# Optimization experiments

Hardware: AMD Instinct MI355X
Metric: run time of the kernel (lower is better)

## Reference

```python
import jax, jax.numpy as jnp
import numpy as np

B, N, H, F, DIN, NC = 4, 1024, 8, 256, 256, 10  # batch graphs, nodes, heads, feat/head, input dim, classes


def setup_inputs() -> dict:
    key = jax.random.key(0)
    ks = jax.random.split(key, 12)
    def rn(k, shape, s=0.05):
        return jax.random.normal(k, shape, jnp.float32) * s
    return dict(
        features=rn(ks[0], (B, N, DIN), 1.0),
        eigvects=rn(ks[1], (B, N, DIN), 1.0),  # unused by forward, mirrors original signature
        attn_mask=jnp.zeros((B, N, N), jnp.float32),  # additive mask: 0 = edge, -inf = no edge
        W1=rn(ks[2], (DIN, H * F)), a_src1=rn(ks[3], (H, F)), a_tgt1=rn(ks[4], (H, F)),
        skip1=rn(ks[5], (DIN, H * F)), b1=jnp.zeros((H * F,), jnp.float32),
        W2=rn(ks[6], (H * F, H * F)), a_src2=rn(ks[7], (H, F)), a_tgt2=rn(ks[8], (H, F)),
        skip2=rn(ks[9], (H * F, H * F)), b2=jnp.zeros((F,), jnp.float32),
        Wc=rn(ks[10], (F, NC)), bc=jnp.zeros((NC,), jnp.float32),
    )


def _gat_layer(x, mask, W, a_s, a_t, skipW, b, concat):
    # GAT IMP2: dense all-pairs scores + additive connectivity mask. Dropout is eval-mode identity.
    Bb, Nn, _ = x.shape
    Hh, Ff = a_s.shape
    p = (x @ W).reshape(Bb, Nn, Hh, Ff)                      # projected node features (B,N,H,F)
    s_src = jnp.einsum('bnhf,hf->bnh', p, a_s)
    s_tgt = jnp.einsum('bnhf,hf->bnh', p, a_t)
    # score[b,i,j,h] = leaky(src_i + tgt_j) + mask[b,i,j]
    scores = jax.nn.leaky_relu(s_src[:, :, None, :] + s_tgt[:, None, :, :], 0.2) + mask[..., None]
    attn = jax.nn.softmax(scores, axis=2)                    # softmax over neighbors j
    out = jnp.einsum('bijh,bjhf->bihf', attn, p)
    out = out + (x @ skipW).reshape(Bb, Nn, Hh, Ff)          # skip connection (projected)
    out = out.reshape(Bb, Nn, Hh * Ff) if concat else out.mean(axis=2)
    out = out + b
    return jax.nn.elu(out) if concat else out


def reference(features, eigvects, attn_mask, W1, a_src1, a_tgt1, skip1, b1,
              W2, a_src2, a_tgt2, skip2, b2, Wc, bc):
    x = _gat_layer(features, attn_mask, W1, a_src1, a_tgt1, skip1, b1, True)   # (B,N,H*F), ELU
    x = _gat_layer(x, attn_mask, W2, a_src2, a_tgt2, skip2, b2, False)         # (B,N,F), heads averaged
    g = x.mean(axis=1)                                                         # mean pool over nodes
    return g @ Wc + bc                                                         # (B, n_classes)
```

## Files before the change

### kernel.cpp

```cpp
#include <hip/hip_runtime.h>
#include <hip/hip_bf16.h>
#include <stdint.h>
#include <stddef.h>

typedef __hip_bfloat16 bf16;
typedef __attribute__((ext_vector_type(8))) short bhalf8;
typedef __attribute__((ext_vector_type(4))) short short4v;
typedef __attribute__((ext_vector_type(4))) float floatx4;

static __device__ __forceinline__ float b2f(bf16 v) { return __bfloat162float(v); }
static __device__ __forceinline__ bf16  f2b(float v) { return __float2bfloat16(v); }
static __device__ __forceinline__ short f2s(float v) {
    union { bf16 b; short s; } u; u.b = __float2bfloat16(v); return u.s;
}
static __device__ __forceinline__ float s2f(short v) {
    union { short s; bf16 b; } u; u.s = v; return b2f(u.b);
}

static __device__ __forceinline__ float loadf(const void* p, size_t i, int f32) {
    return f32 ? ((const float*)p)[i] : b2f(((const bf16*)p)[i]);
}

static __device__ __forceinline__ void gl_lds16(const void* g, void* l) {
    __builtin_amdgcn_global_load_lds(
        (const __attribute__((address_space(1))) void*)g,
        (__attribute__((address_space(3))) void*)l, 16, 0, 0);
}

static __device__ __forceinline__ void load_mask4(const void* mask, size_t idx,
                                                  int f32, float* mv) {
    if (f32) {
        float4 v = *(const float4*)((const float*)mask + idx);
        mv[0] = v.x; mv[1] = v.y; mv[2] = v.z; mv[3] = v.w;
    } else {
        const bf16* p = (const bf16*)mask + idx;
        #pragma unroll
        for (int t = 0; t < 4; t++) mv[t] = b2f(p[t]);
    }
}

__global__ __launch_bounds__(256) void prep_k(const void* __restrict__ feat,
                                              bf16* __restrict__ featc,
                                              float* __restrict__ zbase, int nzero,
                                              const void* __restrict__ W1,
                                              bf16* __restrict__ W1t,
                                              const void* __restrict__ skip1,
                                              bf16* __restrict__ S1t,
                                              const void* __restrict__ W2,
                                              const void* __restrict__ a_src1,
                                              const void* __restrict__ a_tgt1,
                                              const void* __restrict__ a_src2,
                                              const void* __restrict__ a_tgt2,
                                              bf16* __restrict__ Wa1b,
                                              bf16* __restrict__ Wa2b,
                                              int* __restrict__ flagp)
{
    __shared__ int sflag;
    __shared__ bf16 tile[32][33];
    const int tid = threadIdx.x;

    if (tid < 64) {
        const unsigned short* s = (const unsigned short*)W1;
        int bad = 0;
        #pragma unroll
        for (int i = 0; i < 4; i++) {
            int e = (s[tid * 4 + i] >> 7) & 0xFF;
            if (e > 0x85 || (e != 0 && e < 0x60)) bad++;
        }
        bad += __shfl_xor(bad, 1, 64);
        bad += __shfl_xor(bad, 2, 64);
        bad += __shfl_xor(bad, 4, 64);
        bad += __shfl_xor(bad, 8, 64);
        bad += __shfl_xor(bad, 16, 64);
        bad += __shfl_xor(bad, 32, 64);
        if (tid == 0) sflag = (bad > 16) ? 1 : 0;
    }
    __syncthreads();
    const int f32 = sflag;

    int id = blockIdx.x;
    if (id == 0 && tid == 0) *flagp = f32;

    if (id < 4096) {
        const int i = id * 256 + tid;
        featc[i] = f32 ? f2b(((const float*)feat)[i]) : ((const bf16*)feat)[i];
        return;
    }
    id -= 4096;
    if (id < 480) {
        const int i = id * 256 + tid;
        if (i < nzero) zbase[i] = 0.f;
        return;
    }
    id -= 480;
    if (id < 1024) {
        const void* in = (id < 512) ? W1 : skip1;
        bf16* out = (id < 512) ? W1t : S1t;
        const int t = id & 511;
        const int bx = t & 63, byy = t >> 6;
        const int tx = tid & 31, ty = tid >> 5;
        const int c0 = bx * 32, r0 = byy * 32;
        #pragma unroll
        for (int yy = ty; yy < 32; yy += 8)
            tile[yy][tx] = f2b(loadf(in, (size_t)(r0 + yy) * 2048 + c0 + tx, f32));
        __syncthreads();
        #pragma unroll
        for (int yy = ty; yy < 32; yy += 8)
            out[(size_t)(c0 + yy) * 256 + r0 + tx] = tile[tx][yy];
        return;
    }
    id -= 1024;
    if (id < 128) {
        const int wave = tid >> 6, lane = tid & 63;
        const int base = id * 256;
        const int hh = base >> 11, h = hh & 7;
        const void* a = (hh < 8) ? a_src2 : a_tgt2;
        float av[4];
        #pragma unroll
        for (int i = 0; i < 4; i++) av[i] = loadf(a, h * 256 + lane * 4 + i, f32);
        for (int o = 0; o < 64; o++) {
            const int idx = base + wave * 64 + o;
            const int k = idx & 2047;
            float acc = 0.f;
            #pragma unroll
            for (int i = 0; i < 4; i++)
                acc = fmaf(loadf(W2, (size_t)k * 2048 + h * 256 + lane * 4 + i, f32),
                           av[i], acc);
            #pragma unroll
            for (int off2 = 32; off2; off2 >>= 1) acc += __shfl_down(acc, off2, 64);
            if (lane == 0) Wa2b[idx] = f2b(acc);
        }
        return;
    }
    id -= 128;
    {
        const int wave = tid >> 6, lane = tid & 63;
        const int base = id * 256;
        const int hh = base >> 8, h = hh & 7;
        const void* a = (hh < 8) ? a_src1 : a_tgt1;
        float av[4];
        #pragma unroll
        for (int i = 0; i < 4; i++) av[i] = loadf(a, h * 256 + lane * 4 + i, f32);
        for (int o = 0; o < 64; o++) {
            const int idx = base + wave * 64 + o;
            const int k = idx & 255;
            float acc = 0.f;
            #pragma unroll
            for (int i = 0; i < 4; i++)
                acc = fmaf(loadf(W1, (size_t)k * 2048 + h * 256 + lane * 4 + i, f32),
                           av[i], acc);
            #pragma unroll
            for (int off2 = 32; off2; off2 >>= 1) acc += __shfl_down(acc, off2, 64);
            if (lane == 0) Wa1b[idx] = f2b(acc);
        }
    }
}

__global__ __launch_bounds__(256) void gemm_dual(const bf16* __restrict__ featc,
                                                 const bf16* __restrict__ W1t,
                                                 const bf16* __restrict__ S1t,
                                                 bf16* __restrict__ pT,
                                                 bf16* __restrict__ sk1)
{
    __shared__ __align__(16) short sA[128][32];
    __shared__ __align__(16) short sB[128][32];
    const int tid = threadIdx.x;
    const int z = blockIdx.z;
    const bf16* A  = z ? featc : W1t;
    const bf16* Bt = z ? S1t   : featc;
    const int mbase = (z ? blockIdx.x : blockIdx.y) * 128;
    const int nbase = (z ? blockIdx.y : blockIdx.x) * 128;
    const int wave = tid >> 6, lane = tid & 63;
    const int wm = wave >> 1, wn = wave & 1;
    const int lrow = lane & 15, quad = lane >> 4;

    floatx4 acc[4][4];
    #pragma unroll
    for (int i = 0; i < 4; i++)
        #pragma unroll
        for (int j = 0; j < 4; j++)
            acc[i][j] = (floatx4){0.f, 0.f, 0.f, 0.f};

    const int srow = wave * 32 + (lane >> 2);
    const int scol = (lane & 3) * 8;
    const bf16* gA0 = A  + (size_t)(mbase + srow) * 256 + scol;
    const bf16* gA1 = gA0 + (size_t)16 * 256;
    const bf16* gB0 = Bt + (size_t)(nbase + srow) * 256 + scol;
    const bf16* gB1 = gB0 + (size_t)16 * 256;
    char* lA0 = (char*)&sA[0][0] + wave * 2048 + lane * 16;
    char* lA1 = lA0 + 1024;
    char* lB0 = (char*)&sB[0][0] + wave * 2048 + lane * 16;
    char* lB1 = lB0 + 1024;

    for (int k0 = 0; k0 < 256; k0 += 32) {
        __syncthreads();
        gl_lds16(gA0 + k0, lA0);
        gl_lds16(gA1 + k0, lA1);
        gl_lds16(gB0 + k0, lB0);
        gl_lds16(gB1 + k0, lB1);
        __syncthreads();
        bhalf8 af[4], bfr[4];
        #pragma unroll
        for (int t = 0; t < 4; t++) af[t]  = *(const bhalf8*)&sA[wm * 64 + t * 16 + lrow][quad * 8];
        #pragma unroll
        for (int t = 0; t < 4; t++) bfr[t] = *(const bhalf8*)&sB[wn * 64 + t * 16 + lrow][quad * 8];
        #pragma unroll
        for (int tm = 0; tm < 4; tm++)
            #pragma unroll
            for (int tn = 0; tn < 4; tn++)
                acc[tm][tn] = __builtin_amdgcn_mfma_f32_16x16x32_bf16(af[tm], bfr[tn], acc[tm][tn], 0, 0, 0);
    }

    #pragma unroll
    for (int tm = 0; tm < 4; tm++) {
        #pragma unroll
        for (int tn = 0; tn < 4; tn++) {
            const int col = nbase + wn * 64 + tn * 16 + lrow;
            #pragma unroll
            for (int r = 0; r < 4; r++) {
                const int row = mbase + wm * 64 + tm * 16 + quad * 4 + r;
                if (z) {
                    sk1[(size_t)row * 2048 + col] = f2b(acc[tm][tn][r]);
                } else {
                    const size_t idx = ((size_t)((col >> 10) * 8 + (row >> 8)) << 18)
                                     + (size_t)(row & 255) * 1024 + (col & 1023);
                    pT[idx] = f2b(acc[tm][tn][r]);
                }
            }
        }
    }
}

template <int K>
__global__ __launch_bounds__(256) void score_k(const bf16* __restrict__ X,
                                               const bf16* __restrict__ Wab,
                                               float* __restrict__ ss,
                                               float* __restrict__ st)
{
    constexpr int VPL = K / 64;
    const int wave = threadIdx.x >> 6, lane = threadIdx.x & 63;
    const int n = blockIdx.x * 4 + wave;
    const int b = n >> 10, nn = n & 1023;

    const bf16* xr = X + (size_t)n * K + lane * VPL;
    float xv[VPL];
    if (VPL == 4) {
        short4v v = *(const short4v*)xr;
        #pragma unroll
        for (int t = 0; t < 4; t++) xv[t] = s2f(v[t]);
    } else {
        #pragma unroll
        for (int c = 0; c < VPL / 8; c++) {
            bhalf8 v = *(const bhalf8*)(xr + c * 8);
            #pragma unroll
            for (int t = 0; t < 8; t++) xv[c * 8 + t] = s2f(v[t]);
        }
    }

    #pragma unroll
    for (int hh = 0; hh < 16; hh++) {
        const bf16* wr = Wab + (size_t)hh * K + lane * VPL;
        float acc = 0.f;
        if (VPL == 4) {
            short4v v = *(const short4v*)wr;
            #pragma unroll
            for (int t = 0; t < 4; t++) acc = fmaf(xv[t], s2f(v[t]), acc);
        } else {
            #pragma unroll
            for (int c = 0; c < VPL / 8; c++) {
                bhalf8 v = *(const bhalf8*)(wr + c * 8);
                #pragma unroll
                for (int t = 0; t < 8; t++) acc = fmaf(xv[c * 8 + t], s2f(v[t]), acc);
            }
        }
        #pragma unroll
        for (int off = 32; off; off >>= 1) acc += __shfl_down(acc, off, 64);
        if (lane == 0) {
            const int h = hh & 7;
            if (hh < 8) ss[(b * 8 + h) * 1024 + nn] = acc;
            else        st[(b * 8 + h) * 1024 + nn] = acc;
        }
    }
}

__global__ __launch_bounds__(256) void attn_fused(const float* __restrict__ s_src_t,
                                                  const float* __restrict__ s_tgt_t,
                                                  const void* __restrict__ mask,
                                                  const bf16* __restrict__ pT,
                                                  const bf16* __restrict__ sk,
                                                  const void* __restrict__ bias,
                                                  bf16* __restrict__ x2,
                                                  const int* __restrict__ flag)
{
    __shared__ __align__(16) short sA[2][32][32];
    __shared__ __align__(16) short sB[2][256][32];
    __shared__ short sStgt[1024];
    __shared__ float sInvl[32];

    const int tid = threadIdx.x;
    const int by = blockIdx.x, bh = blockIdx.y;
    const int b = bh >> 3, h = bh & 7;
    const int f32 = *flag;
    const int wave = tid >> 6, lane = tid & 63;
    const int lrow = lane & 15, quad = lane >> 4;

    #pragma unroll
    for (int q = 0; q < 4; q++)
        sStgt[q * 256 + tid] = f2s(s_tgt_t[bh * 1024 + q * 256 + tid]);

    const int row  = tid >> 3;
    const int col0 = (tid & 7) * 4;
    const float ssr = s_src_t[bh * 1024 + by * 32 + row];
    const size_t mrow0 = ((size_t)(b * 1024 + by * 32 + row)) << 10;

    const bf16* gB = pT + ((size_t)bh << 18) + (size_t)(tid >> 2) * 1024 + (tid & 3) * 8;

    floatx4 acc[2][4];
    #pragma unroll
    for (int i = 0; i < 2; i++)
        #pragma unroll
        for (int j = 0; j < 4; j++)
            acc[i][j] = (floatx4){0.f, 0.f, 0.f, 0.f};

    float lacc = 0.f;

    auto stageB = [&](int k0, int buf) {
        const bf16* g = gB + k0;
        char* l = (char*)&sB[buf][0][0] + tid * 16;
        #pragma unroll
        for (int c = 0; c < 4; c++)
            gl_lds16(g + (size_t)(64 * c) * 1024, l + c * 4096);
    };
    auto genA = [&](int k0, int buf, const float* mv) {
        const short* sp = &sStgt[k0 + col0];
        short4v ev;
        #pragma unroll
        for (int t = 0; t < 4; t++) {
            float x = ssr + s2f(sp[t]);
            x = fmaxf(x, 0.2f * x);
            float e = __expf(x + mv[t]);
            lacc += e;
            ev[t] = f2s(e);
        }
        *(short4v*)&sA[buf][row][col0] = ev;
    };

    float mv[4];
    stageB(0, 0);
    load_mask4(mask, mrow0 + col0, f32, mv);
    __syncthreads();
    genA(0, 0, mv);
    load_mask4(mask, mrow0 + 32 + col0, f32, mv);

    int cur = 0;
    for (int k0 = 0; k0 < 1024; k0 += 32, cur ^= 1) {
        __syncthreads();
        if (k0 + 32 < 1024) {
            const int nxt = cur ^ 1;
            stageB(k0 + 32, nxt);
            genA(k0 + 32, nxt, mv);
            if (k0 + 64 < 1024)
                load_mask4(mask, mrow0 + k0 + 64 + col0, f32, mv);
        }
        bhalf8 af[2], bfr[4];
        #pragma unroll
        for (int mt = 0; mt < 2; mt++)
            af[mt] = *(const bhalf8*)&sA[cur][mt * 16 + lrow][quad * 8];
        #pragma unroll
        for (int nt = 0; nt < 4; nt++)
            bfr[nt] = *(const bhalf8*)&sB[cur][wave * 64 + nt * 16 + lrow][quad * 8];
        #pragma unroll
        for (int mt = 0; mt < 2; mt++)
            #pragma unroll
            for (int nt = 0; nt < 4; nt++)
                acc[mt][nt] = __builtin_amdgcn_mfma_f32_16x16x32_bf16(af[mt], bfr[nt], acc[mt][nt], 0, 0, 0);
    }

    lacc += __shfl_xor(lacc, 1, 64);
    lacc += __shfl_xor(lacc, 2, 64);
    lacc += __shfl_xor(lacc, 4, 64);
    if ((tid & 7) == 0) sInvl[row] = 1.0f / lacc;
    __syncthreads();

    #pragma unroll
    for (int mt = 0; mt < 2; mt++) {
        #pragma unroll
        for (int r = 0; r < 4; r++) {
            const int rl = mt * 16 + quad * 4 + r;
            const int rg = by * 32 + rl;
            const float il = sInvl[rl];
            #pragma unroll
            for (int nt = 0; nt < 4; nt++) {
                const int col = wave * 64 + nt * 16 + lrow;
                const int hf = h * 256 + col;
                const size_t idx = ((size_t)(b * 1024 + rg)) * 2048 + hf;
                float v = acc[mt][nt][r] * il + b2f(sk[idx]) + loadf(bias, hf, f32);
                v = (v > 0.f) ? v : expm1f(v);
                x2[idx] = f2b(v);
            }
        }
    }
}

__global__ __launch_bounds__(256) void colsoft_k(const float* __restrict__ s_src_t,
                                                 const float* __restrict__ s_tgt_t,
                                                 const void* __restrict__ mask,
                                                 float* __restrict__ c,
                                                 const int* __restrict__ flagp)
{
    __shared__ float sS[64];
    __shared__ float sIl[64];
    const int f32 = *flagp;
    const int bh = blockIdx.x, iz = blockIdx.y, b = bh >> 3;
    const int tid = threadIdx.x;
    const int i0 = iz * 64;
    if (tid < 64) sS[tid] = s_src_t[bh * 1024 + i0 + tid];
    __syncthreads();

    {
        const int row = tid >> 2, c4 = tid & 3;
        const float ssr = sS[row];
        const size_t mrow = ((size_t)(b * 1024 + i0 + row)) << 10;
        float l = 0.f;
        #pragma unroll 4
        for (int q = 0; q < 64; q++) {
            const int j = c4 * 256 + q * 4;
            float mv[4];
            load_mask4(mask, mrow + j, f32, mv);
            float4 s4 = *(const float4*)(s_tgt_t + bh * 1024 + j);
            float sv[4] = {s4.x, s4.y, s4.z, s4.w};
            #pragma unroll
            for (int t = 0; t < 4; t++) {
                float x = ssr + sv[t];
                x = fmaxf(x, 0.2f * x);
                l += __expf(x + mv[t]);
            }
        }
        l += __shfl_xor(l, 1, 64);
        l += __shfl_xor(l, 2, 64);
        if ((tid & 3) == 0) sIl[row] = 1.0f / l;
    }
    __syncthreads();

    const int j0 = tid * 4;
    float4 s4 = *(const float4*)(s_tgt_t + bh * 1024 + j0);
    float sv[4] = {s4.x, s4.y, s4.z, s4.w};
    float a[4] = {0.f, 0.f, 0.f, 0.f};
    #pragma unroll 4
    for (int r = 0; r < 64; r++) {
        const float sr = sS[r], il = sIl[r];
        float mv[4];
        load_mask4(mask, (((size_t)(b * 1024 + i0 + r)) << 10) + j0, f32, mv);
        #pragma unroll
        for (int t = 0; t < 4; t++) {
            float x = sr + sv[t];
            x = fmaxf(x, 0.2f * x);
            a[t] = fmaf(il, __expf(x + mv[t]), a[t]);
        }
    }
    #pragma unroll
    for (int t = 0; t < 4; t++)
        atomicAdd(&c[bh * 1024 + j0 + t], a[t]);
}

__global__ __launch_bounds__(256) void yx_k(const bf16* __restrict__ x2,
                                            const float* __restrict__ c,
                                            float* __restrict__ y,
                                            float* __restrict__ xbar)
{
    __shared__ float sC[8][128];
    const int b = blockIdx.x, kt = blockIdx.y, jc = blockIdx.z;
    const int t = threadIdx.x;
    const int k = kt * 256 + t;
    const int j0 = jc * 128;
    for (int idx = t; idx < 8 * 128; idx += 256) {
        const int h = idx >> 7, jj = idx & 127;
        sC[h][jj] = c[(b * 8 + h) * 1024 + j0 + jj];
    }
    __syncthreads();
    float acc[8] = {0.f, 0.f, 0.f, 0.f, 0.f, 0.f, 0.f, 0.f};
    float ax = 0.f;
    for (int jj = 0; jj < 128; jj++) {
        const float xv = b2f(x2[((size_t)(b * 1024 + j0 + jj)) * 2048 + k]);
        ax += xv;
        #pragma unroll
        for (int h = 0; h < 8; h++) acc[h] = fmaf(sC[h][jj], xv, acc[h]);
    }
    #pragma unroll
    for (int h = 0; h < 8; h++)
        atomicAdd(&y[(b * 8 + h) * 2048 + k], acc[h]);
    atomicAdd(&xbar[b * 2048 + k], ax);
}

__global__ __launch_bounds__(256) void gs_k(const void* __restrict__ W2,
                                            const void* __restrict__ skip2,
                                            const float* __restrict__ y,
                                            const float* __restrict__ xbar,
                                            float* __restrict__ gA,
                                            float* __restrict__ gS,
                                            const int* __restrict__ flagp)
{
    __shared__ float sY[256];
    const int f32 = *flagp;
    int id = blockIdx.x;
    if (id < 256) {
        const int bh = id & 31, kc = id >> 5;
        const int h = bh & 7, f = threadIdx.x;
        const int k0 = kc * 256;
        sY[threadIdx.x] = y[bh * 2048 + k0 + threadIdx.x];
        __syncthreads();
        float acc = 0.f;
        #pragma unroll 4
        for (int kk = 0; kk < 256; kk++)
            acc = fmaf(sY[kk], loadf(W2, (size_t)(k0 + kk) * 2048 + h * 256 + f, f32), acc);
        atomicAdd(&gA[bh * 256 + f], acc);
    } else {
        const int idx = id - 256;
        const int b = idx & 3, hft = (idx >> 2) & 7, kc = idx >> 5;
        const int hf = hft * 256 + threadIdx.x;
        float acc = 0.f;
        #pragma unroll 4
        for (int kk = 0; kk < 256; kk++) {
            const int k = kc * 256 + kk;
            acc = fmaf(xbar[b * 2048 + k], loadf(skip2, (size_t)k * 2048 + hf, f32), acc);
        }
        atomicAdd(&gS[b * 2048 + hf], acc);
    }
}

__global__ __launch_bounds__(256) void classify2_k(const float* __restrict__ gA,
                                                   const float* __restrict__ gS,
                                                   const void* __restrict__ b2,
                                                   const void* __restrict__ Wc,
                                                   const void* __restrict__ bc,
                                                   void* __restrict__ out,
                                                   const int* __restrict__ flag)
{
    __shared__ float gv[256];
    const int f32 = *flag;
    const int b = blockIdx.x, f = threadIdx.x;
    float s = 0.f;
    #pragma unroll
    for (int h = 0; h < 8; h++)
        s += gA[(b * 8 + h) * 256 + f] + gS[b * 2048 + h * 256 + f];
    gv[f] = s * (1.0f / 8192.0f) + loadf(b2, f, f32);
    __syncthreads();
    if (f < 10) {
        float acc = loadf(bc, f, f32);
        for (int k = 0; k < 256; k++)
            acc = fmaf(gv[k], loadf(Wc, k * 10 + f, f32), acc);
        if (f32) ((float*)out)[b * 10 + f] = acc;
        else     ((bf16*)out)[b * 10 + f] = f2b(acc);
    }
}

extern "C" void kernel_launch(void* const* d_in, const int* in_sizes, int n_in,
                              void* d_out, int out_size, void* d_ws, size_t ws_size,
                              hipStream_t stream)
{
    (void)in_sizes; (void)n_in; (void)out_size; (void)ws_size;
    const void* feat   = d_in[0];
    const void* mask   = d_in[2];
    const void* W1     = d_in[3];
    const void* a_src1 = d_in[4];
    const void* a_tgt1 = d_in[5];
    const void* skip1  = d_in[6];
    const void* b1     = d_in[7];
    const void* W2     = d_in[8];
    const void* a_src2 = d_in[9];
    const void* a_tgt2 = d_in[10];
    const void* skip2  = d_in[11];
    const void* b2v    = d_in[12];
    const void* Wc     = d_in[13];
    const void* bc     = d_in[14];

    char* ws = (char*)d_ws;
    size_t off = 0;
    auto alloc = [&](size_t bytes) -> void* {
        void* p = ws + off;
        off += (bytes + 255) & ~(size_t)255;
        return p;
    };
    int*   flag  = (int*)alloc(256);
    bf16*  featc = (bf16*)alloc(4096ull * 256 * 2);
    bf16*  W1t   = (bf16*)alloc(2048ull * 256 * 2);
    bf16*  S1t   = (bf16*)alloc(2048ull * 256 * 2);
    bf16*  sk1   = (bf16*)alloc(4096ull * 2048 * 2);
    bf16*  x2    = (bf16*)alloc(4096ull * 2048 * 2);
    bf16*  pT    = (bf16*)alloc(4096ull * 2048 * 2);
    float* ss    = (float*)alloc(32ull * 1024 * 4);
    float* st    = (float*)alloc(32ull * 1024 * 4);
    bf16*  Wa1b  = (bf16*)alloc(16ull * 256 * 2);
    bf16*  Wa2b  = (bf16*)alloc(16ull * 2048 * 2);
    float* cbuf = (float*)alloc(32ull * 1024 * 4);
    float* gA   = (float*)alloc(32ull * 256 * 4);
    float* gS   = (float*)alloc(4ull * 2048 * 4);
    float* xbar = (float*)alloc(4ull * 2048 * 4);
    float* y    = (float*)alloc(32ull * 2048 * 4);
    const int nzero = 32768 + 3 * 8192 + 65536;

    prep_k<<<5744, 256, 0, stream>>>(feat, featc, cbuf, nzero, W1, W1t,
                                     skip1, S1t, W2, a_src1, a_tgt1,
                                     a_src2, a_tgt2, Wa1b, Wa2b, flag);
    gemm_dual<<<dim3(32, 16, 2), 256, 0, stream>>>(featc, W1t, S1t, pT, sk1);
    score_k<256><<<1024, 256, 0, stream>>>(featc, Wa1b, ss, st);
    attn_fused<<<dim3(32, 32), 256, 0, stream>>>(ss, st, mask, pT, sk1, b1, x2, flag);
    score_k<2048><<<1024, 256, 0, stream>>>(x2, Wa2b, ss, st);
    colsoft_k<<<dim3(32, 16), 256, 0, stream>>>(ss, st, mask, cbuf, flag);
    yx_k<<<dim3(4, 8, 8), 256, 0, stream>>>(x2, cbuf, y, xbar);
    gs_k<<<512, 256, 0, stream>>>(W2, skip2, y, xbar, gA, gS, flag);
    classify2_k<<<4, 256, 0, stream>>>(gA, gS, b2v, Wc, bc, d_out, flag);
}
```

Baseline: 400.0 us.

## Pre-convert mask to bf16 and widen grids for prep, yx and gs kernels

Adds a prep stage that converts the additive mask to a bf16 copy, so attn_fused and colsoft_k read it with 8-byte vector loads and half the bytes, with no runtime dtype branch. The Wa1/Wa2 precompute, yx_k and gs_k are split into more blocks over smaller chunks to raise parallelism on long serial loops. gs_k now stages xbar in shared memory. In exchange there is an extra full pass over the mask in prep and more atomicAdd traffic from the finer splits.

After: 350.0 us. -12.5%, faster.

```diff
diff --git a/kernel.cpp b/kernel.cpp
--- a/kernel.cpp
+++ b/kernel.cpp
@@ -27,20 +27,17 @@
         (__attribute__((address_space(3))) void*)l, 16, 0, 0);
 }
 
-static __device__ __forceinline__ void load_mask4(const void* mask, size_t idx,
-                                                  int f32, float* mv) {
-    if (f32) {
-        float4 v = *(const float4*)((const float*)mask + idx);
-        mv[0] = v.x; mv[1] = v.y; mv[2] = v.z; mv[3] = v.w;
-    } else {
-        const bf16* p = (const bf16*)mask + idx;
-        #pragma unroll
-        for (int t = 0; t < 4; t++) mv[t] = b2f(p[t]);
-    }
+static __device__ __forceinline__ void load_mask4b(const bf16* m, size_t idx,
+                                                   float* mv) {
+    short4v v = *(const short4v*)(m + idx);
+    #pragma unroll
+    for (int t = 0; t < 4; t++) mv[t] = s2f(v[t]);
 }
 
 __global__ __launch_bounds__(256) void prep_k(const void* __restrict__ feat,
                                               bf16* __restrict__ featc,
+                                              const void* __restrict__ mask,
+                                              bf16* __restrict__ maskb,
                                               float* __restrict__ zbase, int nzero,
                                               const void* __restrict__ W1,
                                               bf16* __restrict__ W1t,
@@ -87,6 +84,19 @@
         return;
     }
     id -= 4096;
+    if (id < 4096) {
+        const size_t i = (size_t)id * 1024 + tid * 4;
+        if (f32) {
+            float4 v = *(const float4*)((const float*)mask + i);
+            short4v o;
+            o[0] = f2s(v.x); o[1] = f2s(v.y); o[2] = f2s(v.z); o[3] = f2s(v.w);
+            *(short4v*)(maskb + i) = o;
+        } else {
+            *(short4v*)(maskb + i) = *(const short4v*)((const bf16*)mask + i);
+        }
+        return;
+    }
+    id -= 4096;
     if (id < 480) {
         const int i = id * 256 + tid;
         if (i < nzero) zbase[i] = 0.f;
@@ -110,16 +120,17 @@
         return;
     }
     id -= 1024;
-    if (id < 128) {
+    if (id < 512) {
         const int wave = tid >> 6, lane = tid & 63;
-        const int base = id * 256;
+        const int base = id * 64;
         const int hh = base >> 11, h = hh & 7;
         const void* a = (hh < 8) ? a_src2 : a_tgt2;
         float av[4];
         #pragma unroll
         for (int i = 0; i < 4; i++) av[i] = loadf(a, h * 256 + lane * 4 + i, f32);
-        for (int o = 0; o < 64; o++) {
-            const int idx = base + wave * 64 + o;
+        #pragma unroll 4
+        for (int o = 0; o < 16; o++) {
+            const int idx = base + wave * 16 + o;
             const int k = idx & 2047;
             float acc = 0.f;
             #pragma unroll
@@ -132,17 +143,18 @@
         }
         return;
     }
-    id -= 128;
+    id -= 512;
     {
         const int wave = tid >> 6, lane = tid & 63;
-        const int base = id * 256;
+        const int base = id * 64;
         const int hh = base >> 8, h = hh & 7;
         const void* a = (hh < 8) ? a_src1 : a_tgt1;
         float av[4];
         #pragma unroll
         for (int i = 0; i < 4; i++) av[i] = loadf(a, h * 256 + lane * 4 + i, f32);
-        for (int o = 0; o < 64; o++) {
-            const int idx = base + wave * 64 + o;
+        #pragma unroll 4
+        for (int o = 0; o < 16; o++) {
+            const int idx = base + wave * 16 + o;
             const int k = idx & 255;
             float acc = 0.f;
             #pragma unroll
@@ -285,7 +297,7 @@
 
 __global__ __launch_bounds__(256) void attn_fused(const float* __restrict__ s_src_t,
                                                   const float* __restrict__ s_tgt_t,
-                                                  const void* __restrict__ mask,
+                                                  const bf16* __restrict__ maskb,
                                                   const bf16* __restrict__ pT,
                                                   const bf16* __restrict__ sk,
                                                   const void* __restrict__ bias,
@@ -347,10 +359,10 @@
 
     float mv[4];
     stageB(0, 0);
-    load_mask4(mask, mrow0 + col0, f32, mv);
+    load_mask4b(maskb, mrow0 + col0, mv);
     __syncthreads();
     genA(0, 0, mv);
-    load_mask4(mask, mrow0 + 32 + col0, f32, mv);
+    load_mask4b(maskb, mrow0 + 32 + col0, mv);
 
     int cur = 0;
     for (int k0 = 0; k0 < 1024; k0 += 32, cur ^= 1) {
@@ -360,7 +372,7 @@
             stageB(k0 + 32, nxt);
             genA(k0 + 32, nxt, mv);
             if (k0 + 64 < 1024)
-                load_mask4(mask, mrow0 + k0 + 64 + col0, f32, mv);
+                load_mask4b(maskb, mrow0 + k0 + 64 + col0, mv);
         }
         bhalf8 af[2], bfr[4];
         #pragma unroll
@@ -404,13 +416,11 @@
 
 __global__ __launch_bounds__(256) void colsoft_k(const float* __restrict__ s_src_t,
                                                  const float* __restrict__ s_tgt_t,
-                                                 const void* __restrict__ mask,
-                                                 float* __restrict__ c,
-                                                 const int* __restrict__ flagp)
+                                                 const bf16* __restrict__ maskb,
+                                                 float* __restrict__ c)
 {
     __shared__ float sS[64];
     __shared__ float sIl[64];
-    const int f32 = *flagp;
     const int bh = blockIdx.x, iz = blockIdx.y, b = bh >> 3;
     const int tid = threadIdx.x;
     const int i0 = iz * 64;
@@ -426,7 +436,7 @@
         for (int q = 0; q < 64; q++) {
             const int j = c4 * 256 + q * 4;
             float mv[4];
-            load_mask4(mask, mrow + j, f32, mv);
+            load_mask4b(maskb, mrow + j, mv);
             float4 s4 = *(const float4*)(s_tgt_t + bh * 1024 + j);
             float sv[4] = {s4.x, s4.y, s4.z, s4.w};
             #pragma unroll
@@ -450,7 +460,7 @@
     for (int r = 0; r < 64; r++) {
         const float sr = sS[r], il = sIl[r];
         float mv[4];
-        load_mask4(mask, (((size_t)(b * 1024 + i0 + r)) << 10) + j0, f32, mv);
+        load_mask4b(maskb, (((size_t)(b * 1024 + i0 + r)) << 10) + j0, mv);
         #pragma unroll
         for (int t = 0; t < 4; t++) {
             float x = sr + sv[t];
@@ -468,19 +478,20 @@
                                             float* __restrict__ y,
                                             float* __restrict__ xbar)
 {
-    __shared__ float sC[8][128];
+    __shared__ float sC[8][32];
     const int b = blockIdx.x, kt = blockIdx.y, jc = blockIdx.z;
     const int t = threadIdx.x;
     const int k = kt * 256 + t;
-    const int j0 = jc * 128;
-    for (int idx = t; idx < 8 * 128; idx += 256) {
-        const int h = idx >> 7, jj = idx & 127;
+    const int j0 = jc * 32;
+    {
+        const int h = t >> 5, jj = t & 31;
         sC[h][jj] = c[(b * 8 + h) * 1024 + j0 + jj];
     }
     __syncthreads();
     float acc[8] = {0.f, 0.f, 0.f, 0.f, 0.f, 0.f, 0.f, 0.f};
     float ax = 0.f;
-    for (int jj = 0; jj < 128; jj++) {
+    #pragma unroll 4
+    for (int jj = 0; jj < 32; jj++) {
         const float xv = b2f(x2[((size_t)(b * 1024 + j0 + jj)) * 2048 + k]);
         ax += xv;
         #pragma unroll
@@ -500,30 +511,31 @@
                                             float* __restrict__ gS,
                                             const int* __restrict__ flagp)
 {
-    __shared__ float sY[256];
+    __shared__ float sY[64];
     const int f32 = *flagp;
     int id = blockIdx.x;
-    if (id < 256) {
+    if (id < 1024) {
         const int bh = id & 31, kc = id >> 5;
         const int h = bh & 7, f = threadIdx.x;
-        const int k0 = kc * 256;
-        sY[threadIdx.x] = y[bh * 2048 + k0 + threadIdx.x];
+        const int k0 = kc * 64;
+        if (threadIdx.x < 64) sY[threadIdx.x] = y[bh * 2048 + k0 + threadIdx.x];
         __syncthreads();
         float acc = 0.f;
         #pragma unroll 4
-        for (int kk = 0; kk < 256; kk++)
+        for (int kk = 0; kk < 64; kk++)
             acc = fmaf(sY[kk], loadf(W2, (size_t)(k0 + kk) * 2048 + h * 256 + f, f32), acc);
         atomicAdd(&gA[bh * 256 + f], acc);
     } else {
-        const int idx = id - 256;
+        const int idx = id - 1024;
         const int b = idx & 3, hft = (idx >> 2) & 7, kc = idx >> 5;
         const int hf = hft * 256 + threadIdx.x;
+        const int k0 = kc * 64;
+        if (threadIdx.x < 64) sY[threadIdx.x] = xbar[b * 2048 + k0 + threadIdx.x];
+        __syncthreads();
         float acc = 0.f;
         #pragma unroll 4
-        for (int kk = 0; kk < 256; kk++) {
-            const int k = kc * 256 + kk;
-            acc = fmaf(xbar[b * 2048 + k], loadf(skip2, (size_t)k * 2048 + hf, f32), acc);
-        }
+        for (int kk = 0; kk < 64; kk++)
+            acc = fmaf(sY[kk], loadf(skip2, (size_t)(k0 + kk) * 2048 + hf, f32), acc);
         atomicAdd(&gS[b * 2048 + hf], acc);
     }
 }
@@ -583,6 +595,7 @@
     };
     int*   flag  = (int*)alloc(256);
     bf16*  featc = (bf16*)alloc(4096ull * 256 * 2);
+    bf16*  maskb = (bf16*)alloc(4ull * 1024 * 1024 * 2);
     bf16*  W1t   = (bf16*)alloc(2048ull * 256 * 2);
     bf16*  S1t   = (bf16*)alloc(2048ull * 256 * 2);
     bf16*  sk1   = (bf16*)alloc(4096ull * 2048 * 2);
@@ -599,15 +612,16 @@
     float* y    = (float*)alloc(32ull * 2048 * 4);
     const int nzero = 32768 + 3 * 8192 + 65536;
 
-    prep_k<<<5744, 256, 0, stream>>>(feat, featc, cbuf, nzero, W1, W1t,
-                                     skip1, S1t, W2, a_src1, a_tgt1,
-                                     a_src2, a_tgt2, Wa1b, Wa2b, flag);
+    prep_k<<<10272, 256, 0, stream>>>(feat, featc, mask, maskb, cbuf, nzero,
+                                      W1, W1t, skip1, S1t, W2,
+                                      a_src1, a_tgt1, a_src2, a_tgt2,
+                                      Wa1b, Wa2b, flag);
     gemm_dual<<<dim3(32, 16, 2), 256, 0, stream>>>(featc, W1t, S1t, pT, sk1);
     score_k<256><<<1024, 256, 0, stream>>>(featc, Wa1b, ss, st);
-    attn_fused<<<dim3(32, 32), 256, 0, stream>>>(ss, st, mask, pT, sk1, b1, x2, flag);
+    attn_fused<<<dim3(32, 32), 256, 0, stream>>>(ss, st, maskb, pT, sk1, b1, x2, flag);
     score_k<2048><<<1024, 256, 0, stream>>>(x2, Wa2b, ss, st);
-    colsoft_k<<<dim3(32, 16), 256, 0, stream>>>(ss, st, mask, cbuf, flag);
-    yx_k<<<dim3(4, 8, 8), 256, 0, stream>>>(x2, cbuf, y, xbar);
-    gs_k<<<512, 256, 0, stream>>>(W2, skip2, y, xbar, gA, gS, flag);
+    colsoft_k<<<dim3(32, 16), 256, 0, stream>>>(ss, st, maskb, cbuf);
+    yx_k<<<dim3(4, 8, 32), 256, 0, stream>>>(x2, cbuf, y, xbar);
+    gs_k<<<2048, 256, 0, stream>>>(W2, skip2, y, xbar, gA, gS, flag);
     classify2_k<<<4, 256, 0, stream>>>(gA, gS, b2v, Wc, bc, d_out, flag);
 }
```
